# Kernel optimization log

Hardware: AMD Instinct MI355X
Metric: run time of the kernel (lower is better)

The kernel has to match this reference:

```python
import jax, jax.numpy as jnp
import numpy as np

STRIDES = (8.0, 16.0, 32.0)
REG_MAX = 7
TOP_K = 100          # top_k_n: max per class and max total
NMS_PRE = 1000       # hardcoded prefilter in get_bboxes
IOU_THRES = 0.5      # literal passed to combined_non_max_suppression
BOX_SCORE = 0.3
IMG_SIZE = (640.0, 640.0)


def _centers(h, w, stride):
    # row-major (h, w) flatten, points stored as (y, x)
    y = (jnp.arange(h, dtype=jnp.float32) + 0.5) * stride
    x = (jnp.arange(w, dtype=jnp.float32) + 0.5) * stride
    return jnp.stack([jnp.repeat(y, w), jnp.tile(x, h)], axis=-1)  # [h*w, 2]


def _distribution(bbox_pred, stride):
    # softmax over reg_max+1 bins -> expected distance, scaled by stride
    b = bbox_pred.shape[0]
    p = jax.nn.softmax(bbox_pred.reshape(b, -1, REG_MAX + 1), axis=-1)
    ln = jnp.arange(REG_MAX + 1, dtype=jnp.float32)
    d = jnp.einsum('bnk,k->bn', p, ln).reshape(b, -1, 4)
    return d * stride


def _process_level(cls_score, bbox_pred, stride):
    b, h, w, c = cls_score.shape
    scores = jax.nn.sigmoid(cls_score.reshape(b, h * w, c))
    dist = _distribution(bbox_pred, stride)                     # [b, hw, 4]
    pts = jnp.broadcast_to(_centers(h, w, stride)[None], (b, h * w, 2))
    if h * w > NMS_PRE:  # static shape check, mirrors TF graph specialization
        max_scores = jnp.max(scores, axis=-1)                   # [b, hw]
        _, topk = jax.lax.top_k(max_scores, NMS_PRE)            # [b, NMS_PRE]
        scores = jnp.take_along_axis(scores, topk[..., None], axis=1)
        dist = jnp.take_along_axis(dist, topk[..., None], axis=1)
        pts = jnp.take_along_axis(pts, topk[..., None], axis=1)
    # distance2bbox with clipping to model input shape
    y1 = jnp.clip(pts[..., 0] - dist[..., 0], 0.0, IMG_SIZE[0])
    x1 = jnp.clip(pts[..., 1] - dist[..., 1], 0.0, IMG_SIZE[1])
    y2 = jnp.clip(pts[..., 0] + dist[..., 2], 0.0, IMG_SIZE[0])
    x2 = jnp.clip(pts[..., 1] + dist[..., 3], 0.0, IMG_SIZE[1])
    return jnp.stack([y1, x1, y2, x2], axis=-1), scores


def _iou_1_vs_n(box, boxes):
    yy1 = jnp.maximum(box[0], boxes[:, 0])
    xx1 = jnp.maximum(box[1], boxes[:, 1])
    yy2 = jnp.minimum(box[2], boxes[:, 2])
    xx2 = jnp.minimum(box[3], boxes[:, 3])
    inter = jnp.maximum(yy2 - yy1, 0.0) * jnp.maximum(xx2 - xx1, 0.0)
    a1 = (box[2] - box[0]) * (box[3] - box[1])
    a2 = (boxes[:, 2] - boxes[:, 0]) * (boxes[:, 3] - boxes[:, 1])
    return inter / (a1 + a2 - inter + 1e-9)


def _nms_single(boxes, scores):
    # greedy NMS, fixed TOP_K iterations; boxes [N,4], scores [N]
    def step(s, _):
        i = jnp.argmax(s)
        sc = s[i]
        suppress = _iou_1_vs_n(boxes[i], boxes) > IOU_THRES
        s = jnp.where(suppress, -jnp.inf, s)
        s = s.at[i].set(-jnp.inf)
        return s, (i, sc)
    _, (idx, sel) = jax.lax.scan(step, scores, None, length=TOP_K)
    return idx, sel  # [TOP_K] each


def _combined_nms(boxes, scores):
    # per-class NMS then global top-K, emulating tf.image.combined_non_max_suppression
    n, c = scores.shape
    idx, sel = jax.vmap(_nms_single, in_axes=(None, 1))(boxes, scores)  # [C, K]
    sel_boxes = boxes[idx]                                              # [C, K, 4]
    cls = jnp.broadcast_to(jnp.arange(c, dtype=jnp.float32)[:, None], (c, TOP_K))
    flat_s = sel.reshape(-1)
    flat_s = jnp.where(jnp.isfinite(flat_s), flat_s, -1.0)
    top_s, top_i = jax.lax.top_k(flat_s, TOP_K)
    out_boxes = sel_boxes.reshape(-1, 4)[top_i]
    out_cls = cls.reshape(-1)[top_i]
    ok = top_s > -1.0
    out_s = jnp.where(ok, top_s, 0.0)
    out_boxes = jnp.where(ok[:, None], out_boxes, 0.0)
    out_cls = jnp.where(ok, out_cls, 0.0)
    return out_boxes, out_s, out_cls


def setup_inputs() -> dict:
    key = jax.random.key(0)
    ks = jax.random.split(key, 7)
    b, c = 16, 20
    inp = {}
    for i, hw in enumerate((80, 40, 20)):
        inp[f'cls_score_{i}'] = jax.random.normal(ks[i], (b, hw, hw, c), dtype=jnp.float32)
        inp[f'bbox_pred_{i}'] = jax.random.normal(ks[3 + i], (b, hw, hw, 4 * (REG_MAX + 1)), dtype=jnp.float32)
    inp['origin_shapes'] = jax.random.uniform(ks[6], (b, 2), dtype=jnp.float32) * 1280.0
    return inp


def reference(cls_score_0, cls_score_1, cls_score_2,
              bbox_pred_0, bbox_pred_1, bbox_pred_2, origin_shapes):
    cls_scores = (cls_score_0, cls_score_1, cls_score_2)
    bbox_preds = (bbox_pred_0, bbox_pred_1, bbox_pred_2)
    mlvl_b, mlvl_s = [], []
    for cs, bp, st in zip(cls_scores, bbox_preds, STRIDES):
        bb, sc = _process_level(cs, bp, st)
        mlvl_b.append(bb)
        mlvl_s.append(sc)
    boxes = jnp.concatenate(mlvl_b, axis=1)    # [B, 2400, 4]
    scores = jnp.concatenate(mlvl_s, axis=1)   # [B, 2400, C]
    nb, ns, nc = jax.vmap(_combined_nms)(boxes, scores)
    out = jnp.concatenate([nb, ns[..., None], nc[..., None]], axis=-1)  # [B, K, 6]
    mask = (ns > BOX_SCORE).astype(out.dtype)
    return out * mask[..., None]
```

## Files before the change

### kernel.cpp

```cpp
#include <hip/hip_runtime.h>
#include <math.h>

#define BATCH 16
#define NCLS 20
#define TOPK 100
#define NPRE 1000
#define NTOT 2400
#define NBINS 8
#define N0 6400
#define N1 1600
#define SSEL 256

#define MID05 0.50000002980232238769531250

__device__ __forceinline__ unsigned int orderable(float x) {
    unsigned int u = __float_as_uint(x);
    return (u & 0x80000000u) ? ~u : (u | 0x80000000u);
}
__device__ __forceinline__ float unorderable(unsigned int k) {
    return __uint_as_float((k & 0x80000000u) ? (k ^ 0x80000000u) : ~k);
}

__device__ __forceinline__ void radix_pass_scan(
        const unsigned int* hist, unsigned int* s_prefix, unsigned int* s_kk,
        unsigned int prefix, unsigned int kk, int t) {
    if (t < 64) {
        uint4 h = *(const uint4*)&hist[t * 4];
        unsigned int s3 = h.w;
        unsigned int s2 = h.z + s3;
        unsigned int s1 = h.y + s2;
        unsigned int s0 = h.x + s1;
        unsigned int S = s0;
        #pragma unroll
        for (int off = 1; off < 64; off <<= 1) {
            unsigned int o = __shfl_down(S, off);
            S += (t + off < 64) ? o : 0u;
        }
        unsigned int Sgt = S - s0;
        unsigned int F0 = s0 + Sgt, F1 = s1 + Sgt, F2 = s2 + Sgt, F3 = s3 + Sgt;
        if (F0 >= kk && F1 < kk)  { *s_prefix = (prefix << 8) | (unsigned int)(t * 4 + 0); *s_kk = kk - F1; }
        if (F1 >= kk && F2 < kk)  { *s_prefix = (prefix << 8) | (unsigned int)(t * 4 + 1); *s_kk = kk - F2; }
        if (F2 >= kk && F3 < kk)  { *s_prefix = (prefix << 8) | (unsigned int)(t * 4 + 2); *s_kk = kk - F3; }
        if (F3 >= kk && Sgt < kk) { *s_prefix = (prefix << 8) | (unsigned int)(t * 4 + 3); *s_kk = kk - Sgt; }
    }
}

__device__ __forceinline__ unsigned long long bmerge_shfl(
        unsigned long long v, int t, int k2, int jmax) {
    for (int j2 = jmax; j2 > 0; j2 >>= 1) {
        unsigned long long o = __shfl_xor(v, j2);
        bool km = (((t & k2) == 0) == ((t & j2) != 0));
        v = km ? (v > o ? v : o) : (v < o ? v : o);
    }
    return v;
}

__global__ __launch_bounds__(256) void compute_keys_kernel(
        const float* __restrict__ cls0, const float* __restrict__ cls1,
        unsigned int* __restrict__ keys0, unsigned int* __restrict__ keys1) {
    int tg = blockIdx.x * 256 + threadIdx.x;
    const float* p;
    unsigned int* dst;
    if (tg < BATCH * N0) {
        p = cls0 + (size_t)tg * NCLS;
        dst = keys0 + tg;
    } else {
        int a = tg - BATCH * N0;
        if (a >= BATCH * N1) return;
        p = cls1 + (size_t)a * NCLS;
        dst = keys1 + a;
    }
    const float4* p4 = (const float4*)p;
    float m = -INFINITY;
    #pragma unroll
    for (int q = 0; q < 5; ++q) {
        float4 v = p4[q];
        m = fmaxf(m, fmaxf(fmaxf(v.x, v.y), fmaxf(v.z, v.w)));
    }
    *dst = orderable(m);
}

__global__ __launch_bounds__(256) void radix_select_kernel(
        const unsigned int* __restrict__ keys0, const unsigned int* __restrict__ keys1,
        int* __restrict__ sel_idx) {
    int bid = blockIdx.x;
    int b = bid >> 1;
    int lvl = bid & 1;
    int n = (lvl == 0) ? N0 : N1;
    const unsigned int* gk = (lvl == 0 ? keys0 : keys1) + (size_t)b * n;

    __shared__ unsigned int skey[N0];
    __shared__ __align__(16) unsigned int hist[256];
    __shared__ int eq[256];
    __shared__ unsigned int s_prefix, s_kk, s_cnt, s_eqcnt;
    int t = threadIdx.x;

    for (int a = t; a < n; a += 256) skey[a] = gk[a];
    if (t == 0) { s_kk = NPRE; s_prefix = 0u; s_cnt = 0u; s_eqcnt = 0u; }
    __syncthreads();

    for (int pass = 0; pass < 4; ++pass) {
        int shift = 24 - 8 * pass;
        unsigned int prefix = s_prefix, kk = s_kk;
        hist[t] = 0u;
        __syncthreads();
        for (int a = t; a < n; a += 256) {
            unsigned int u = skey[a];
            if (pass == 0 || (u >> (shift + 8)) == prefix)
                atomicAdd(&hist[(u >> shift) & 255u], 1u);
        }
        __syncthreads();
        radix_pass_scan(hist, &s_prefix, &s_kk, prefix, kk, t);
        __syncthreads();
    }

    unsigned int T = s_prefix;
    int* out = sel_idx + b * 2000 + lvl * 1000;
    for (int a = t; a < n; a += 256) {
        unsigned int u = skey[a];
        if (u > T) {
            unsigned int pos = atomicAdd(&s_cnt, 1u);
            out[pos] = a;
        } else if (u == T) {
            unsigned int p = atomicAdd(&s_eqcnt, 1u);
            if (p < 256u) eq[p] = a;
        }
    }
    __syncthreads();
    if (t == 0) {
        unsigned int pos = s_cnt;
        unsigned int rem = s_kk;
        unsigned int cnt = s_eqcnt;
        if (cnt <= 256u) {
            for (unsigned int i = 1; i < cnt; ++i) {
                int key = eq[i]; int j2 = (int)i - 1;
                while (j2 >= 0 && eq[j2] > key) { eq[j2 + 1] = eq[j2]; --j2; }
                eq[j2 + 1] = key;
            }
            for (unsigned int i = 0; i < rem; ++i) out[pos + i] = eq[i];
        } else {
            for (int a = 0; a < n && rem > 0u; ++a)
                if (skey[a] == T) { out[pos++] = a; --rem; }
        }
    }
}

__global__ __launch_bounds__(256) void decode_kernel(
        const float* __restrict__ cls0, const float* __restrict__ cls1, const float* __restrict__ cls2,
        const float* __restrict__ bb0,  const float* __restrict__ bb1,  const float* __restrict__ bb2,
        const int* __restrict__ sel_idx,
        float* __restrict__ boxes_all, float* __restrict__ scores_t) {
    int tg = blockIdx.x * blockDim.x + threadIdx.x;
    if (tg >= BATCH * NTOT) return;
    int b = tg / NTOT, j = tg % NTOT;

    const float* cls; const float* bb; int a, w; float stride;
    if (j < 1000) {
        a = sel_idx[b * 2000 + j]; w = 80; stride = 8.f;
        cls = cls0 + ((size_t)b * N0 + a) * NCLS;
        bb  = bb0  + ((size_t)b * N0 + a) * 32;
    } else if (j < 2000) {
        a = sel_idx[b * 2000 + j]; w = 40; stride = 16.f;
        cls = cls1 + ((size_t)b * N1 + a) * NCLS;
        bb  = bb1  + ((size_t)b * N1 + a) * 32;
    } else {
        a = j - 2000; w = 20; stride = 32.f;
        cls = cls2 + ((size_t)b * 400 + a) * NCLS;
        bb  = bb2  + ((size_t)b * 400 + a) * 32;
    }

    float cl[20];
    {
        const float4* c4 = (const float4*)cls;
        #pragma unroll
        for (int q = 0; q < 5; ++q) *(float4*)&cl[q * 4] = c4[q];
    }
    float bl[32];
    {
        const float4* b4 = (const float4*)bb;
        #pragma unroll
        for (int q = 0; q < 8; ++q) *(float4*)&bl[q * 4] = b4[q];
    }

    #pragma unroll
    for (int c = 0; c < NCLS; ++c)
        scores_t[((size_t)b * NCLS + c) * NTOT + j] = 1.f / (1.f + expf(-cl[c]));

    float d[4];
    #pragma unroll
    for (int s = 0; s < 4; ++s) {
        const float* l = &bl[s * NBINS];
        float m = l[0];
        #pragma unroll
        for (int k = 1; k < NBINS; ++k) m = fmaxf(m, l[k]);
        float e[NBINS], sum = 0.f;
        #pragma unroll
        for (int k = 0; k < NBINS; ++k) { e[k] = expf(l[k] - m); sum += e[k]; }
        float acc = 0.f;
        #pragma unroll
        for (int k = 0; k < NBINS; ++k) acc += (e[k] / sum) * (float)k;
        d[s] = acc * stride;
    }
    float cy = ((float)(a / w) + 0.5f) * stride;
    float cx = ((float)(a % w) + 0.5f) * stride;
    float* bx = boxes_all + ((size_t)b * NTOT + j) * 4;
    bx[0] = fminf(fmaxf(cy - d[0], 0.f), 640.f);
    bx[1] = fminf(fmaxf(cx - d[1], 0.f), 640.f);
    bx[2] = fminf(fmaxf(cy + d[2], 0.f), 640.f);
    bx[3] = fminf(fmaxf(cx + d[3], 0.f), 640.f);
}

__global__ __launch_bounds__(256) void class_nms_kernel(
        const float* __restrict__ boxes_all, const float* __restrict__ scores_t,
        float* __restrict__ nms_score, int* __restrict__ nms_idx) {
    int blk = blockIdx.x;
    int b = blk / NCLS;
    int t = threadIdx.x;

    __shared__ unsigned int skey[NTOT];
    __shared__ __align__(16) unsigned int hist[256];
    __shared__ int eq[128];
    __shared__ unsigned int s_prefix, s_kk, s_cnt, s_eqcnt;
    __shared__ unsigned long long sorted[SSEL];
    __shared__ float4 abox[TOPK];
    __shared__ float4 cbox[64];
    __shared__ int s_outPos;
    __shared__ unsigned long long s_m;

    const float*  ssrc = scores_t + (size_t)blk * NTOT;
    const float4* bsrc = (const float4*)boxes_all + (size_t)b * NTOT;
    float* osc = nms_score + (size_t)blk * TOPK;
    int*   oid = nms_idx   + (size_t)blk * TOPK;

    for (int j = t; j < NTOT; j += 256) skey[j] = orderable(ssrc[j]);
    if (t == 0) { s_kk = SSEL; s_prefix = 0u; s_cnt = 0u; s_eqcnt = 0u; s_outPos = 0; }
    __syncthreads();

    for (int pass = 0; pass < 4; ++pass) {
        int shift = 24 - 8 * pass;
        unsigned int prefix = s_prefix, kk = s_kk;
        hist[t] = 0u;
        __syncthreads();
        for (int j = t; j < NTOT; j += 256) {
            unsigned int u = skey[j];
            if (pass == 0 || (u >> (shift + 8)) == prefix)
                atomicAdd(&hist[(u >> shift) & 255u], 1u);
        }
        __syncthreads();
        radix_pass_scan(hist, &s_prefix, &s_kk, prefix, kk, t);
        __syncthreads();
    }

    unsigned int T = s_prefix;
    for (int j = t; j < NTOT; j += 256) {
        unsigned int u = skey[j];
        if (u > T) {
            unsigned int pos = atomicAdd(&s_cnt, 1u);
            sorted[pos] = ((unsigned long long)u << 32) | (unsigned int)~j;
        } else if (u == T) {
            unsigned int p = atomicAdd(&s_eqcnt, 1u);
            if (p < 128u) eq[p] = j;
        }
    }
    __syncthreads();
    if (t == 0) {
        unsigned int pos = s_cnt;
        unsigned int rem = s_kk;
        unsigned int cnt = s_eqcnt;
        if (cnt <= 128u) {
            for (unsigned int i = 1; i < cnt; ++i) {
                int key = eq[i]; int j2 = (int)i - 1;
                while (j2 >= 0 && eq[j2] > key) { eq[j2 + 1] = eq[j2]; --j2; }
                eq[j2 + 1] = key;
            }
            for (unsigned int i = 0; i < rem; ++i)
                sorted[pos + i] = ((unsigned long long)T << 32) | (unsigned int)~eq[i];
        } else {
            for (int j = 0; j < NTOT && rem > 0u; ++j)
                if (skey[j] == T) {
                    sorted[pos++] = ((unsigned long long)T << 32) | (unsigned int)~j;
                    --rem;
                }
        }
    }
    __syncthreads();

    {
        unsigned long long v = sorted[t];
        #pragma unroll
        for (int k2 = 2; k2 <= 64; k2 <<= 1)
            v = bmerge_shfl(v, t, k2, k2 >> 1);
        sorted[t] = v;
        __syncthreads();
        {
            unsigned long long o = sorted[t ^ 64];
            bool km = (((t & 128) == 0) == ((t & 64) != 0));
            v = km ? (v > o ? v : o) : (v < o ? v : o);
            v = bmerge_shfl(v, t, 128, 32);
        }
        __syncthreads();
        sorted[t] = v;
        __syncthreads();
        {
            unsigned long long o = sorted[t ^ 128];
            bool km = ((t & 128) != 0);
            v = km ? (v > o ? v : o) : (v < o ? v : o);
        }
        __syncthreads();
        sorted[t] = v;
        __syncthreads();
        {
            unsigned long long o = sorted[t ^ 64];
            bool km = ((t & 64) != 0);
            v = km ? (v > o ? v : o) : (v < o ? v : o);
            v = bmerge_shfl(v, t, 256, 32);
        }
        __syncthreads();
        sorted[t] = v;
        __syncthreads();
    }

    if (t < 64) {
        int lane = t;
        int outPos = 0;
        for (int chunk = 0; chunk < SSEL / 64 && outPos < TOPK; ++chunk) {
            unsigned long long key = sorted[SSEL - 1 - (chunk * 64 + lane)];
            unsigned int j = ~(unsigned int)key;
            float sc = unorderable((unsigned int)(key >> 32));
            float4 bj = bsrc[j];
            cbox[lane] = bj;
            float amine = (bj.z - bj.x) * (bj.w - bj.y);

            bool sup = false;
            for (int t2 = 0; t2 < outPos; ++t2) {
                float4 wb = abox[t2];
                float a1 = (wb.z - wb.x) * (wb.w - wb.y);
                float yy1 = fmaxf(wb.x, bj.x);
                float xx1 = fmaxf(wb.y, bj.y);
                float yy2 = fminf(wb.z, bj.z);
                float xx2 = fminf(wb.w, bj.w);
                float inter = fmaxf(yy2 - yy1, 0.f) * fmaxf(xx2 - xx1, 0.f);
                float denom = a1 + amine - inter + 1e-9f;
                sup = sup || ((double)inter > MID05 * (double)denom);
            }

            unsigned long long supmask = 0ull;
            #pragma unroll 8
            for (int j2 = 0; j2 < 64; ++j2) {
                float4 wb = cbox[j2];
                float a1 = (wb.z - wb.x) * (wb.w - wb.y);
                float yy1 = fmaxf(wb.x, bj.x);
                float xx1 = fmaxf(wb.y, bj.y);
                float yy2 = fminf(wb.z, bj.z);
                float xx2 = fminf(wb.w, bj.w);
                float inter = fmaxf(yy2 - yy1, 0.f) * fmaxf(xx2 - xx1, 0.f);
                float denom = a1 + amine - inter + 1e-9f;
                bool s2 = ((double)inter > MID05 * (double)denom);
                if (s2 && j2 < lane) supmask |= (1ull << j2);
            }

            unsigned long long cand = __ballot(!sup);
            unsigned long long accbits = 0ull;
            while (cand) {
                int i = __builtin_ctzll(cand);
                accbits |= (1ull << i);
                cand &= ~(1ull << i);
                unsigned long long row = __ballot((supmask >> i) & 1ull);
                cand &= ~row;
            }

            int nAcc = (int)__builtin_popcountll(accbits);
            int avail = TOPK - outPos;
            bool mine = (accbits >> lane) & 1ull;
            int myrank = (int)__builtin_popcountll(accbits & ((1ull << lane) - 1ull));
            if (mine && myrank < avail) {
                int pos = outPos + myrank;
                osc[pos] = sc;
                oid[pos] = (int)j;
                abox[pos] = bj;
            }
            outPos += (nAcc < avail) ? nAcc : avail;
            __builtin_amdgcn_s_waitcnt(0);
        }
        if (lane == 0) s_outPos = outPos;
    }
    __syncthreads();

    int outPos = s_outPos;
    if (outPos < TOPK) {
        if (t < SSEL) skey[~(unsigned int)sorted[t]] = 0u;
        __syncthreads();
        for (int j = t; j < NTOT; j += 256) {
            unsigned int u = skey[j];
            if (!u) continue;
            float4 bj = bsrc[j];
            float amine = (bj.z - bj.x) * (bj.w - bj.y);
            bool sup = false;
            for (int t2 = 0; t2 < outPos; ++t2) {
                float4 wb = abox[t2];
                float a1 = (wb.z - wb.x) * (wb.w - wb.y);
                float yy1 = fmaxf(wb.x, bj.x);
                float xx1 = fmaxf(wb.y, bj.y);
                float yy2 = fminf(wb.z, bj.z);
                float xx2 = fminf(wb.w, bj.w);
                float inter = fmaxf(yy2 - yy1, 0.f) * fmaxf(xx2 - xx1, 0.f);
                float denom = a1 + amine - inter + 1e-9f;
                sup = sup || ((double)inter > MID05 * (double)denom);
            }
            if (sup) skey[j] = 0u;
        }
        __syncthreads();
        while (outPos < TOPK) {
            if (t == 0) s_m = 0ull;
            __syncthreads();
            unsigned long long loc = 0ull;
            for (int j = t; j < NTOT; j += 256) {
                unsigned int u = skey[j];
                if (u) {
                    unsigned long long kk = ((unsigned long long)u << 32) | (unsigned int)~j;
                    loc = (kk > loc) ? kk : loc;
                }
            }
            atomicMax(&s_m, loc);
            __syncthreads();
            unsigned long long m = s_m;
            if ((long long)m >= 0) break;
            unsigned int wi = ~(unsigned int)m;
            float4 wb = bsrc[wi];
            if (t == 0) {
                osc[outPos] = unorderable((unsigned int)(m >> 32));
                oid[outPos] = (int)wi;
                skey[wi] = 0u;
            }
            __syncthreads();
            float a1 = (wb.z - wb.x) * (wb.w - wb.y);
            for (int j = t; j < NTOT; j += 256) {
                unsigned int u = skey[j];
                if (!u) continue;
                float4 bj = bsrc[j];
                float yy1 = fmaxf(wb.x, bj.x);
                float xx1 = fmaxf(wb.y, bj.y);
                float yy2 = fminf(wb.z, bj.z);
                float xx2 = fminf(wb.w, bj.w);
                float inter = fmaxf(yy2 - yy1, 0.f) * fmaxf(xx2 - xx1, 0.f);
                float a2 = (bj.z - bj.x) * (bj.w - bj.y);
                float denom = a1 + a2 - inter + 1e-9f;
                if ((double)inter > MID05 * (double)denom) skey[j] = 0u;
            }
            ++outPos;
            __syncthreads();
        }
    }

    for (int k2 = outPos + t; k2 < TOPK; k2 += 256) { osc[k2] = -INFINITY; oid[k2] = 0; }
}

__global__ __launch_bounds__(256) void final_topk_kernel(
        const float* __restrict__ nms_score, const int* __restrict__ nms_idx,
        const float* __restrict__ boxes_all, float* __restrict__ out) {
    int b = blockIdx.x, t = threadIdx.x;
    __shared__ unsigned int fkey[2000];
    __shared__ __align__(16) unsigned int hist[256];
    __shared__ int eq[128];
    __shared__ unsigned long long fk[128];
    __shared__ unsigned int s_prefix, s_kk, s_cnt, s_eqcnt;

    for (int f = t; f < 2000; f += 256) {
        float s = nms_score[(size_t)b * 2000 + f];
        float v = isfinite(s) ? s : -1.0f;
        fkey[f] = orderable(v);
    }
    if (t == 0) { s_kk = TOPK; s_prefix = 0u; s_cnt = 0u; s_eqcnt = 0u; }
    if (t < 128) fk[t] = 0ull;
    __syncthreads();

    for (int pass = 0; pass < 4; ++pass) {
        int shift = 24 - 8 * pass;
        unsigned int prefix = s_prefix, kk = s_kk;
        hist[t] = 0u;
        __syncthreads();
        for (int f = t; f < 2000; f += 256) {
            unsigned int u = fkey[f];
            if (pass == 0 || (u >> (shift + 8)) == prefix)
                atomicAdd(&hist[(u >> shift) & 255u], 1u);
        }
        __syncthreads();
        radix_pass_scan(hist, &s_prefix, &s_kk, prefix, kk, t);
        __syncthreads();
    }

    unsigned int T = s_prefix;
    for (int f = t; f < 2000; f += 256) {
        unsigned int u = fkey[f];
        if (u > T) {
            unsigned int pos = atomicAdd(&s_cnt, 1u);
            fk[pos] = ((unsigned long long)u << 32) | (unsigned int)~f;
        } else if (u == T) {
            unsigned int p = atomicAdd(&s_eqcnt, 1u);
            if (p < 128u) eq[p] = f;
        }
    }
    __syncthreads();
    if (t == 0) {
        unsigned int pos = s_cnt;
        unsigned int rem = s_kk;
        unsigned int cnt = s_eqcnt;
        if (cnt <= 128u) {
            for (unsigned int i = 1; i < cnt; ++i) {
                int key = eq[i]; int j2 = (int)i - 1;
                while (j2 >= 0 && eq[j2] > key) { eq[j2 + 1] = eq[j2]; --j2; }
                eq[j2 + 1] = key;
            }
            for (unsigned int i = 0; i < rem; ++i)
                fk[pos + i] = ((unsigned long long)T << 32) | (unsigned int)~eq[i];
        } else {
            for (int f = 0; f < 2000 && rem > 0u; ++f)
                if (fkey[f] == T) {
                    fk[pos++] = ((unsigned long long)T << 32) | (unsigned int)~f;
                    --rem;
                }
        }
    }
    __syncthreads();

    {
        unsigned long long v = (t < 128) ? fk[t] : 0ull;
        if (t < 128) {
            #pragma unroll
            for (int k2 = 2; k2 <= 64; k2 <<= 1)
                v = bmerge_shfl(v, t, k2, k2 >> 1);
            fk[t] = v;
        }
        __syncthreads();
        if (t < 128) {
            unsigned long long o = fk[t ^ 64];
            bool km = ((t & 64) != 0);
            v = km ? (v > o ? v : o) : (v < o ? v : o);
            v = bmerge_shfl(v, t, 128, 32);
        }
        __syncthreads();
        if (t < 128) fk[t] = v;
        __syncthreads();
    }

    if (t < TOPK) {
        unsigned long long kk = fk[127 - t];
        float v = unorderable((unsigned int)(kk >> 32));
        int fi = (int)~(unsigned int)kk;
        float* o = out + ((size_t)b * TOPK + t) * 6;
        if (v > 0.3f) {
            int bidx = nms_idx[(size_t)b * 2000 + fi];
            float4 bxw = ((const float4*)boxes_all)[(size_t)b * NTOT + bidx];
            o[0] = bxw.x; o[1] = bxw.y; o[2] = bxw.z; o[3] = bxw.w;
            o[4] = v; o[5] = (float)(fi / TOPK);
        } else {
            o[0] = 0.f; o[1] = 0.f; o[2] = 0.f; o[3] = 0.f; o[4] = 0.f; o[5] = 0.f;
        }
    }
}

extern "C" void kernel_launch(void* const* d_in, const int* in_sizes, int n_in,
                              void* d_out, int out_size, void* d_ws, size_t ws_size,
                              hipStream_t stream) {
    (void)out_size; (void)ws_size;
    const float* cls[3] = {nullptr, nullptr, nullptr};
    const float* bbx[3] = {nullptr, nullptr, nullptr};
    for (int i = 0; i < n_in; ++i) {
        const float* p = (const float*)d_in[i];
        switch (in_sizes[i]) {
            case 16 * 6400 * 20: cls[0] = p; break;
            case 16 * 6400 * 32: bbx[0] = p; break;
            case 16 * 1600 * 20: cls[1] = p; break;
            case 16 * 1600 * 32: bbx[1] = p; break;
            case 16 *  400 * 20: cls[2] = p; break;
            case 16 *  400 * 32: bbx[2] = p; break;
            default: break;
        }
    }

    char* w = (char*)d_ws;
    int*   sel_idx    = (int*)(w);
    float* boxes_all  = (float*)(w + 131072);
    float* scores_t   = (float*)(w + 745472);
    unsigned int* keys0 = (unsigned int*)(w + 745472);
    unsigned int* keys1 = (unsigned int*)(w + 745472 + 409600);
    float* nms_score  = (float*)(w + 3817472);
    int*   nms_idx    = (int*)(w + 3945472);

    hipLaunchKernelGGL(compute_keys_kernel, dim3((BATCH * (N0 + N1) + 255) / 256), dim3(256), 0, stream,
                       cls[0], cls[1], keys0, keys1);
    hipLaunchKernelGGL(radix_select_kernel, dim3(32), dim3(256), 0, stream,
                       keys0, keys1, sel_idx);
    hipLaunchKernelGGL(decode_kernel, dim3((BATCH * NTOT + 255) / 256), dim3(256), 0, stream,
                       cls[0], cls[1], cls[2], bbx[0], bbx[1], bbx[2],
                       sel_idx, boxes_all, scores_t);
    hipLaunchKernelGGL(class_nms_kernel, dim3(BATCH * NCLS), dim3(256), 0, stream,
                       boxes_all, scores_t, nms_score, nms_idx);
    hipLaunchKernelGGL(final_topk_kernel, dim3(BATCH), dim3(256), 0, stream,
                       nms_score, nms_idx, boxes_all, (float*)d_out);
}
```

Measured before the change: 153.5 us.

## Fuse key computation into radix select and final top-k into class NMS

Removes the separate key-computation kernel: the radix-select kernel now runs 1024 threads per block and computes per-anchor max-class keys straight from the class scores into shared memory. The final top-k kernel is folded into the class NMS kernel, where the last-finishing class block for each batch, found with an atomic counter and thread fences, does the cross-class top-k. This removes two kernel launches and the global round-trip for the keys. In exchange only 32 blocks now read the large level-0 score tensor, and a per-batch counter is added that must be reset on every call.

```diff
diff --git a/kernel.cpp b/kernel.cpp
--- a/kernel.cpp
+++ b/kernel.cpp
@@ -55,39 +55,14 @@
     return v;
 }
 
-__global__ __launch_bounds__(256) void compute_keys_kernel(
+__global__ __launch_bounds__(1024) void select_keys_kernel(
         const float* __restrict__ cls0, const float* __restrict__ cls1,
-        unsigned int* __restrict__ keys0, unsigned int* __restrict__ keys1) {
-    int tg = blockIdx.x * 256 + threadIdx.x;
-    const float* p;
-    unsigned int* dst;
-    if (tg < BATCH * N0) {
-        p = cls0 + (size_t)tg * NCLS;
-        dst = keys0 + tg;
-    } else {
-        int a = tg - BATCH * N0;
-        if (a >= BATCH * N1) return;
-        p = cls1 + (size_t)a * NCLS;
-        dst = keys1 + a;
-    }
-    const float4* p4 = (const float4*)p;
-    float m = -INFINITY;
-    #pragma unroll
-    for (int q = 0; q < 5; ++q) {
-        float4 v = p4[q];
-        m = fmaxf(m, fmaxf(fmaxf(v.x, v.y), fmaxf(v.z, v.w)));
-    }
-    *dst = orderable(m);
-}
-
-__global__ __launch_bounds__(256) void radix_select_kernel(
-        const unsigned int* __restrict__ keys0, const unsigned int* __restrict__ keys1,
-        int* __restrict__ sel_idx) {
+        int* __restrict__ sel_idx, int* __restrict__ cnt) {
     int bid = blockIdx.x;
     int b = bid >> 1;
     int lvl = bid & 1;
     int n = (lvl == 0) ? N0 : N1;
-    const unsigned int* gk = (lvl == 0 ? keys0 : keys1) + (size_t)b * n;
+    const float* cls = (lvl == 0 ? cls0 : cls1) + (size_t)b * (size_t)n * NCLS;
 
     __shared__ unsigned int skey[N0];
     __shared__ __align__(16) unsigned int hist[256];
@@ -95,16 +70,27 @@
     __shared__ unsigned int s_prefix, s_kk, s_cnt, s_eqcnt;
     int t = threadIdx.x;
 
-    for (int a = t; a < n; a += 256) skey[a] = gk[a];
+    if (bid == 0 && t < BATCH) cnt[t] = 0;
+
+    for (int a = t; a < n; a += 1024) {
+        const float4* p4 = (const float4*)(cls + (size_t)a * NCLS);
+        float m = -INFINITY;
+        #pragma unroll
+        for (int q = 0; q < 5; ++q) {
+            float4 v = p4[q];
+            m = fmaxf(m, fmaxf(fmaxf(v.x, v.y), fmaxf(v.z, v.w)));
+        }
+        skey[a] = orderable(m);
+    }
     if (t == 0) { s_kk = NPRE; s_prefix = 0u; s_cnt = 0u; s_eqcnt = 0u; }
     __syncthreads();
 
     for (int pass = 0; pass < 4; ++pass) {
         int shift = 24 - 8 * pass;
         unsigned int prefix = s_prefix, kk = s_kk;
-        hist[t] = 0u;
-        __syncthreads();
-        for (int a = t; a < n; a += 256) {
+        if (t < 256) hist[t] = 0u;
+        __syncthreads();
+        for (int a = t; a < n; a += 1024) {
             unsigned int u = skey[a];
             if (pass == 0 || (u >> (shift + 8)) == prefix)
                 atomicAdd(&hist[(u >> shift) & 255u], 1u);
@@ -116,7 +102,7 @@
 
     unsigned int T = s_prefix;
     int* out = sel_idx + b * 2000 + lvl * 1000;
-    for (int a = t; a < n; a += 256) {
+    for (int a = t; a < n; a += 1024) {
         unsigned int u = skey[a];
         if (u > T) {
             unsigned int pos = atomicAdd(&s_cnt, 1u);
@@ -130,9 +116,9 @@
     if (t == 0) {
         unsigned int pos = s_cnt;
         unsigned int rem = s_kk;
-        unsigned int cnt = s_eqcnt;
-        if (cnt <= 256u) {
-            for (unsigned int i = 1; i < cnt; ++i) {
+        unsigned int cnt2 = s_eqcnt;
+        if (cnt2 <= 256u) {
+            for (unsigned int i = 1; i < cnt2; ++i) {
                 int key = eq[i]; int j2 = (int)i - 1;
                 while (j2 >= 0 && eq[j2] > key) { eq[j2 + 1] = eq[j2]; --j2; }
                 eq[j2 + 1] = key;
@@ -212,7 +198,8 @@
 
 __global__ __launch_bounds__(256) void class_nms_kernel(
         const float* __restrict__ boxes_all, const float* __restrict__ scores_t,
-        float* __restrict__ nms_score, int* __restrict__ nms_idx) {
+        float* __restrict__ nms_score, int* __restrict__ nms_idx,
+        int* __restrict__ cnt, float* __restrict__ outbuf) {
     int blk = blockIdx.x;
     int b = blk / NCLS;
     int t = threadIdx.x;
@@ -226,6 +213,7 @@
     __shared__ float4 cbox[64];
     __shared__ int s_outPos;
     __shared__ unsigned long long s_m;
+    __shared__ int s_last;
 
     const float*  ssrc = scores_t + (size_t)blk * NTOT;
     const float4* bsrc = (const float4*)boxes_all + (size_t)b * NTOT;
@@ -266,9 +254,9 @@
     if (t == 0) {
         unsigned int pos = s_cnt;
         unsigned int rem = s_kk;
-        unsigned int cnt = s_eqcnt;
-        if (cnt <= 128u) {
-            for (unsigned int i = 1; i < cnt; ++i) {
+        unsigned int cnt2 = s_eqcnt;
+        if (cnt2 <= 128u) {
+            for (unsigned int i = 1; i < cnt2; ++i) {
                 int key = eq[i]; int j2 = (int)i - 1;
                 while (j2 >= 0 && eq[j2] > key) { eq[j2 + 1] = eq[j2]; --j2; }
                 eq[j2 + 1] = key;
@@ -453,25 +441,24 @@
     }
 
     for (int k2 = outPos + t; k2 < TOPK; k2 += 256) { osc[k2] = -INFINITY; oid[k2] = 0; }
-}
-
-__global__ __launch_bounds__(256) void final_topk_kernel(
-        const float* __restrict__ nms_score, const int* __restrict__ nms_idx,
-        const float* __restrict__ boxes_all, float* __restrict__ out) {
-    int b = blockIdx.x, t = threadIdx.x;
-    __shared__ unsigned int fkey[2000];
-    __shared__ __align__(16) unsigned int hist[256];
-    __shared__ int eq[128];
-    __shared__ unsigned long long fk[128];
-    __shared__ unsigned int s_prefix, s_kk, s_cnt, s_eqcnt;
+
+    __syncthreads();
+    if (t == 0) {
+        __threadfence();
+        int old = atomicAdd(&cnt[b], 1);
+        s_last = (old == NCLS - 1) ? 1 : 0;
+        if (s_last) __threadfence();
+    }
+    __syncthreads();
+    if (!s_last) return;
 
     for (int f = t; f < 2000; f += 256) {
         float s = nms_score[(size_t)b * 2000 + f];
         float v = isfinite(s) ? s : -1.0f;
-        fkey[f] = orderable(v);
+        skey[f] = orderable(v);
     }
     if (t == 0) { s_kk = TOPK; s_prefix = 0u; s_cnt = 0u; s_eqcnt = 0u; }
-    if (t < 128) fk[t] = 0ull;
+    if (t < 128) sorted[t] = 0ull;
     __syncthreads();
 
     for (int pass = 0; pass < 4; ++pass) {
@@ -480,7 +467,7 @@
         hist[t] = 0u;
         __syncthreads();
         for (int f = t; f < 2000; f += 256) {
-            unsigned int u = fkey[f];
+            unsigned int u = skey[f];
             if (pass == 0 || (u >> (shift + 8)) == prefix)
                 atomicAdd(&hist[(u >> shift) & 255u], 1u);
         }
@@ -489,13 +476,13 @@
         __syncthreads();
     }
 
-    unsigned int T = s_prefix;
+    unsigned int Tf = s_prefix;
     for (int f = t; f < 2000; f += 256) {
-        unsigned int u = fkey[f];
-        if (u > T) {
+        unsigned int u = skey[f];
+        if (u > Tf) {
             unsigned int pos = atomicAdd(&s_cnt, 1u);
-            fk[pos] = ((unsigned long long)u << 32) | (unsigned int)~f;
-        } else if (u == T) {
+            sorted[pos] = ((unsigned long long)u << 32) | (unsigned int)~f;
+        } else if (u == Tf) {
             unsigned int p = atomicAdd(&s_eqcnt, 1u);
             if (p < 128u) eq[p] = f;
         }
@@ -504,19 +491,19 @@
     if (t == 0) {
         unsigned int pos = s_cnt;
         unsigned int rem = s_kk;
-        unsigned int cnt = s_eqcnt;
-        if (cnt <= 128u) {
-            for (unsigned int i = 1; i < cnt; ++i) {
+        unsigned int cnt2 = s_eqcnt;
+        if (cnt2 <= 128u) {
+            for (unsigned int i = 1; i < cnt2; ++i) {
                 int key = eq[i]; int j2 = (int)i - 1;
                 while (j2 >= 0 && eq[j2] > key) { eq[j2 + 1] = eq[j2]; --j2; }
                 eq[j2 + 1] = key;
             }
             for (unsigned int i = 0; i < rem; ++i)
-                fk[pos + i] = ((unsigned long long)T << 32) | (unsigned int)~eq[i];
+                sorted[pos + i] = ((unsigned long long)Tf << 32) | (unsigned int)~eq[i];
         } else {
             for (int f = 0; f < 2000 && rem > 0u; ++f)
-                if (fkey[f] == T) {
-                    fk[pos++] = ((unsigned long long)T << 32) | (unsigned int)~f;
+                if (skey[f] == Tf) {
+                    sorted[pos++] = ((unsigned long long)Tf << 32) | (unsigned int)~f;
                     --rem;
                 }
         }
@@ -524,30 +511,30 @@
     __syncthreads();
 
     {
-        unsigned long long v = (t < 128) ? fk[t] : 0ull;
+        unsigned long long v = (t < 128) ? sorted[t] : 0ull;
         if (t < 128) {
             #pragma unroll
             for (int k2 = 2; k2 <= 64; k2 <<= 1)
                 v = bmerge_shfl(v, t, k2, k2 >> 1);
-            fk[t] = v;
+            sorted[t] = v;
         }
         __syncthreads();
         if (t < 128) {
-            unsigned long long o = fk[t ^ 64];
+            unsigned long long o = sorted[t ^ 64];
             bool km = ((t & 64) != 0);
             v = km ? (v > o ? v : o) : (v < o ? v : o);
             v = bmerge_shfl(v, t, 128, 32);
         }
         __syncthreads();
-        if (t < 128) fk[t] = v;
+        if (t < 128) sorted[t] = v;
         __syncthreads();
     }
 
     if (t < TOPK) {
-        unsigned long long kk = fk[127 - t];
+        unsigned long long kk = sorted[127 - t];
         float v = unorderable((unsigned int)(kk >> 32));
         int fi = (int)~(unsigned int)kk;
-        float* o = out + ((size_t)b * TOPK + t) * 6;
+        float* o = outbuf + ((size_t)b * TOPK + t) * 6;
         if (v > 0.3f) {
             int bidx = nms_idx[(size_t)b * 2000 + fi];
             float4 bxw = ((const float4*)boxes_all)[(size_t)b * NTOT + bidx];
@@ -582,20 +569,15 @@
     int*   sel_idx    = (int*)(w);
     float* boxes_all  = (float*)(w + 131072);
     float* scores_t   = (float*)(w + 745472);
-    unsigned int* keys0 = (unsigned int*)(w + 745472);
-    unsigned int* keys1 = (unsigned int*)(w + 745472 + 409600);
     float* nms_score  = (float*)(w + 3817472);
     int*   nms_idx    = (int*)(w + 3945472);
-
-    hipLaunchKernelGGL(compute_keys_kernel, dim3((BATCH * (N0 + N1) + 255) / 256), dim3(256), 0, stream,
-                       cls[0], cls[1], keys0, keys1);
-    hipLaunchKernelGGL(radix_select_kernel, dim3(32), dim3(256), 0, stream,
-                       keys0, keys1, sel_idx);
+    int*   cnt        = (int*)(w + 4073472);
+
+    hipLaunchKernelGGL(select_keys_kernel, dim3(32), dim3(1024), 0, stream,
+                       cls[0], cls[1], sel_idx, cnt);
     hipLaunchKernelGGL(decode_kernel, dim3((BATCH * NTOT + 255) / 256), dim3(256), 0, stream,
                        cls[0], cls[1], cls[2], bbx[0], bbx[1], bbx[2],
                        sel_idx, boxes_all, scores_t);
     hipLaunchKernelGGL(class_nms_kernel, dim3(BATCH * NCLS), dim3(256), 0, stream,
-                       boxes_all, scores_t, nms_score, nms_idx);
-    hipLaunchKernelGGL(final_topk_kernel, dim3(BATCH), dim3(256), 0, stream,
-                       nms_score, nms_idx, boxes_all, (float*)d_out);
-}
+                       boxes_all, scores_t, nms_score, nms_idx, cnt, (float*)d_out);
+}
```

Measured after the change: 154.2 us, median of 2. Within noise of the previous version (+0.5%).
